# Performance work log

Hardware: AMD Instinct MI355X
Metric: run time of the kernel (lower is better)

The kernel has to match this reference:

```python
import jax, jax.numpy as jnp
import numpy as np

NUM_HEADS = 12

def setup_inputs() -> dict:
    key = jax.random.key(0)
    ks = jax.random.split(key, 4)
    B, N, C = 64, 512, 768
    x = jax.random.normal(ks[0], (B, N, C), dtype=jnp.float32)
    qkv_w = jax.random.normal(ks[1], (3 * C, C), dtype=jnp.float32) * 0.02
    proj_w = jax.random.normal(ks[2], (C, C), dtype=jnp.float32) * 0.02
    proj_b = jnp.zeros((C,), dtype=jnp.float32)
    bias_table = jax.random.normal(ks[3], (2 * N - 1, NUM_HEADS), dtype=jnp.float32) * 0.02
    return {"x": x, "qkv_w": qkv_w, "proj_w": proj_w, "proj_b": proj_b, "bias_table": bias_table}

def reference(x, qkv_w, proj_w, proj_b, bias_table):
    B, N, C = x.shape
    H = NUM_HEADS
    hd = C // H
    scale = hd ** (-0.5)
    # qkv projection (no bias): [B,N,3C] -> [3,B,H,N,hd]
    qkv = (x @ qkv_w.T).reshape(B, N, 3, H, hd)
    qkv = jnp.transpose(qkv, (2, 0, 3, 1, 4))
    q, k, v = qkv[0], qkv[1], qkv[2]
    # relative position bias: rel index in [0, 2N-2]
    coords = jnp.arange(N)
    rel = coords[:, None] - coords[None, :] + (N - 1)  # [N,N]
    bias = jnp.transpose(bias_table[rel], (2, 0, 1))   # [H,N,N]
    attn = jnp.einsum('bhnd,bhmd->bhnm', q, k) * scale + bias[None]
    attn = jax.nn.softmax(attn, axis=-1)
    out = jnp.einsum('bhnm,bhmd->bhnd', attn, v)       # [B,H,N,hd]
    out = jnp.transpose(out, (0, 2, 1, 3)).reshape(B, N, C)
    return out @ proj_w.T + proj_b
```

## Files before the change

kernel.cpp:

```cpp
#include <hip/hip_runtime.h>
#include <hip/hip_bf16.h>

#define DI static __device__ __forceinline__

typedef __attribute__((ext_vector_type(8), may_alias)) short short8;
typedef __attribute__((ext_vector_type(4), may_alias)) short short4a;
typedef __attribute__((ext_vector_type(4), may_alias)) float floatx4a;
typedef __attribute__((ext_vector_type(4))) float floatx4;

constexpr int Bsz = 64, Nseq = 512, Cdim = 768, NH = 12, HD = 64;
constexpr int QS = Bsz * NH * Nseq * HD;
constexpr float QK_PRESCALE = 0.18033688011112042f;
constexpr float LOG2E = 1.4426950408889634f;

DI ushort f2bf(float f) {
  union { float f; unsigned u; } v; v.f = f;
  unsigned r = v.u + 0x7FFF + ((v.u >> 16) & 1);
  return (ushort)(r >> 16);
}
DI float bf2f(ushort u) {
  union { unsigned u; float f; } v; v.u = ((unsigned)u) << 16;
  return v.f;
}

DI void gload_lds16(const ushort* g, ushort* l) {
  __builtin_amdgcn_global_load_lds(
      (const __attribute__((address_space(1))) unsigned int*)g,
      (__attribute__((address_space(3))) unsigned int*)l, 16, 0, 0);
}

__global__ void cvt8(const float* __restrict__ s, ushort* __restrict__ d, int n) {
  int i = (blockIdx.x * 256 + threadIdx.x) * 8;
  if (i >= n) return;
  floatx4a a = *(const floatx4a*)(s + i);
  floatx4a b = *(const floatx4a*)(s + i + 4);
  short8 r;
  r[0] = (short)f2bf(a[0]); r[1] = (short)f2bf(a[1]);
  r[2] = (short)f2bf(a[2]); r[3] = (short)f2bf(a[3]);
  r[4] = (short)f2bf(b[0]); r[5] = (short)f2bf(b[1]);
  r[6] = (short)f2bf(b[2]); r[7] = (short)f2bf(b[3]);
  *(short8*)(d + i) = r;
}
__global__ void cvt1s(const float* __restrict__ s, ushort* __restrict__ d, int n) {
  int i = blockIdx.x * 256 + threadIdx.x;
  if (i < n) d[i] = f2bf(s[i] * LOG2E);
}

__global__ __launch_bounds__(256) void qkv_gemm(
    const ushort* __restrict__ x, const ushort* __restrict__ w,
    ushort* __restrict__ qo, ushort* __restrict__ ko, ushort* __restrict__ vo)
{
  __shared__ __align__(16) ushort As[128 * 64];
  __shared__ __align__(16) ushort Ws[128 * 64];
  const int id = blockIdx.y * 18 + blockIdx.x;
  const int swz = (id & 7) * 576 + (id >> 3);
  const int bm = swz / 18;
  const int bn = swz % 18;
  const int t = threadIdx.x;
  const int wv = t >> 6, ln = t & 63, lq = ln >> 4, lm = ln & 15;
  const int wm = wv >> 1, wn = wv & 1;

  const int srow = wv * 32 + (ln >> 3);
  const int scol = (ln & 7) * 8;

  floatx4 acc[4][4];
  #pragma unroll
  for (int i = 0; i < 4; ++i)
    #pragma unroll
    for (int j = 0; j < 4; ++j) acc[i][j] = (floatx4)0.f;

  for (int kt = 0; kt < Cdim / 64; ++kt) {
    #pragma unroll
    for (int i = 0; i < 4; ++i) {
      gload_lds16(&x[(size_t)(bm * 128 + srow + i * 8) * Cdim + kt * 64 + scol],
                  &As[(wv * 32 + i * 8) * 64]);
      gload_lds16(&w[(size_t)(bn * 128 + srow + i * 8) * Cdim + kt * 64 + scol],
                  &Ws[(wv * 32 + i * 8) * 64]);
    }
    __syncthreads();
    #pragma unroll
    for (int ks = 0; ks < 2; ++ks) {
      short8 af[4], bfr[4];
      #pragma unroll
      for (int i = 0; i < 4; ++i)
        af[i] = *(const short8*)&As[(wm * 64 + i * 16 + lm) * 64 + ks * 32 + lq * 8];
      #pragma unroll
      for (int j = 0; j < 4; ++j)
        bfr[j] = *(const short8*)&Ws[(wn * 64 + j * 16 + lm) * 64 + ks * 32 + lq * 8];
      #pragma unroll
      for (int i = 0; i < 4; ++i)
        #pragma unroll
        for (int j = 0; j < 4; ++j)
          acc[i][j] = __builtin_amdgcn_mfma_f32_16x16x32_bf16(af[i], bfr[j], acc[i][j], 0, 0, 0);
    }
    __syncthreads();
  }

  const int cbase = bn * 128 + wn * 64;
  const int which = cbase / Cdim;
  const int h = (cbase % Cdim) >> 6;
  const float osc = (which == 0) ? QK_PRESCALE : 1.f;
  #pragma unroll
  for (int i = 0; i < 4; ++i) {
    int gm0 = bm * 128 + wm * 64 + i * 16 + lq * 4;
    int b = gm0 >> 9, ns0 = gm0 & 511;
    #pragma unroll
    for (int j = 0; j < 4; ++j) {
      int d = j * 16 + lm;
      if (which == 2) {
        short4a v4;
        #pragma unroll
        for (int r = 0; r < 4; ++r) v4[r] = (short)f2bf(acc[i][j][r]);
        *(short4a*)&vo[(size_t)((b * NH + h) * HD + d) * Nseq + ns0] = v4;
      } else {
        ushort* outp = which == 0 ? qo : ko;
        #pragma unroll
        for (int r = 0; r < 4; ++r)
          outp[(size_t)((b * NH + h) * Nseq + ns0 + r) * HD + d] = f2bf(acc[i][j][r] * osc);
      }
    }
  }
}

__global__ __launch_bounds__(256) void attn_kernel(
    const ushort* __restrict__ q, const ushort* __restrict__ k,
    const ushort* __restrict__ vt, const ushort* __restrict__ bt,
    ushort* __restrict__ ao)
{
  __shared__ __align__(16) ushort Qs[64 * 72];
  __shared__ __align__(16) ushort Ks[64 * 72];
  __shared__ __align__(16) ushort Vs[64 * 72];
  __shared__ __align__(16) ushort Ps[64 * 72];
  __shared__ float biasLds[128];
  const int blk = blockIdx.x;
  const int bh = blk % (Bsz * NH);
  const int qt = blk / (Bsz * NH);
  const int h = bh % NH, b = bh / NH;
  const int t = threadIdx.x;
  const int wv = t >> 6, ln = t & 63, lq = ln >> 4, lm = ln & 15;
  const size_t base = (size_t)bh * (Nseq * HD);

  #pragma unroll
  for (int i = 0; i < 2; ++i) {
    int id = t + 256 * i;
    int r = id >> 3, c = (id & 7) << 3;
    *(short8*)&Qs[r * 72 + c] =
        *(const short8*)&q[base + (size_t)(qt * 64 + r) * HD + c];
  }
  __syncthreads();
  short8 qa[2];
  #pragma unroll
  for (int ks = 0; ks < 2; ++ks)
    qa[ks] = *(const short8*)&Qs[(wv * 16 + lm) * 72 + ks * 32 + lq * 8];

  floatx4 o[4];
  #pragma unroll
  for (int i = 0; i < 4; ++i) o[i] = (floatx4)0.f;
  float lrow[4];
  #pragma unroll
  for (int r = 0; r < 4; ++r) lrow[r] = 0.f;

  for (int kt = 0; kt < Nseq / 64; ++kt) {
    #pragma unroll
    for (int i = 0; i < 2; ++i) {
      int id = t + 256 * i;
      int r = id >> 3, c = (id & 7) << 3;
      *(short8*)&Ks[r * 72 + c] =
          *(const short8*)&k[base + (size_t)(kt * 64 + r) * HD + c];
      *(short8*)&Vs[r * 72 + c] =
          *(const short8*)&vt[base + (size_t)r * Nseq + kt * 64 + c];
    }
    if (t < 127) biasLds[t] = bf2f(bt[(qt * 64 - kt * 64 + 448 + t) * NH + h]);
    __syncthreads();

    floatx4 s[4];
    #pragma unroll
    for (int cb = 0; cb < 4; ++cb) s[cb] = (floatx4)0.f;
    #pragma unroll
    for (int ks = 0; ks < 2; ++ks) {
      #pragma unroll
      for (int cb = 0; cb < 4; ++cb) {
        short8 bfr = *(const short8*)&Ks[(cb * 16 + lm) * 72 + ks * 32 + lq * 8];
        s[cb] = __builtin_amdgcn_mfma_f32_16x16x32_bf16(qa[ks], bfr, s[cb], 0, 0, 0);
      }
    }

    #pragma unroll
    for (int r = 0; r < 4; ++r) {
      int row_in = wv * 16 + lq * 4 + r;
      #pragma unroll
      for (int cb = 0; cb < 4; ++cb) {
        int col_in = cb * 16 + lm;
        float p = __builtin_amdgcn_exp2f(s[cb][r] + biasLds[row_in - col_in + 63]);
        lrow[r] += p;
        Ps[row_in * 72 + col_in] = f2bf(p);
      }
    }
    __syncthreads();

    #pragma unroll
    for (int ks = 0; ks < 2; ++ks) {
      short8 a = *(const short8*)&Ps[(wv * 16 + lm) * 72 + ks * 32 + lq * 8];
      #pragma unroll
      for (int db = 0; db < 4; ++db) {
        short8 bfr = *(const short8*)&Vs[(db * 16 + lm) * 72 + ks * 32 + lq * 8];
        o[db] = __builtin_amdgcn_mfma_f32_16x16x32_bf16(a, bfr, o[db], 0, 0, 0);
      }
    }
    __syncthreads();
  }

  #pragma unroll
  for (int r = 0; r < 4; ++r) {
    #pragma unroll
    for (int off = 8; off; off >>= 1) lrow[r] += __shfl_xor(lrow[r], off);
  }

  #pragma unroll
  for (int r = 0; r < 4; ++r) {
    int qi = qt * 64 + wv * 16 + lq * 4 + r;
    float inv = 1.f / lrow[r];
    #pragma unroll
    for (int db = 0; db < 4; ++db) {
      int d = db * 16 + lm;
      ao[(size_t)(b * Nseq + qi) * Cdim + h * HD + d] = f2bf(o[db][r] * inv);
    }
  }
}

__global__ __launch_bounds__(256) void proj_gemm(
    const ushort* __restrict__ a, const ushort* __restrict__ w,
    const ushort* __restrict__ pb, float* __restrict__ out)
{
  __shared__ __align__(16) ushort As[128 * 64];
  __shared__ __align__(16) ushort Ws[128 * 64];
  const int id = blockIdx.y * 6 + blockIdx.x;
  const int swz = (id & 7) * 192 + (id >> 3);
  const int bm = swz / 6;
  const int bn = swz % 6;
  const int t = threadIdx.x;
  const int wv = t >> 6, ln = t & 63, lq = ln >> 4, lm = ln & 15;
  const int wm = wv >> 1, wn = wv & 1;

  const int srow = wv * 32 + (ln >> 3);
  const int scol = (ln & 7) * 8;

  floatx4 acc[4][4];
  #pragma unroll
  for (int i = 0; i < 4; ++i)
    #pragma unroll
    for (int j = 0; j < 4; ++j) acc[i][j] = (floatx4)0.f;

  for (int kt = 0; kt < Cdim / 64; ++kt) {
    #pragma unroll
    for (int i = 0; i < 4; ++i) {
      gload_lds16(&a[(size_t)(bm * 128 + srow + i * 8) * Cdim + kt * 64 + scol],
                  &As[(wv * 32 + i * 8) * 64]);
      gload_lds16(&w[(size_t)(bn * 128 + srow + i * 8) * Cdim + kt * 64 + scol],
                  &Ws[(wv * 32 + i * 8) * 64]);
    }
    __syncthreads();
    #pragma unroll
    for (int ks = 0; ks < 2; ++ks) {
      short8 af[4], bfr[4];
      #pragma unroll
      for (int i = 0; i < 4; ++i)
        af[i] = *(const short8*)&As[(wm * 64 + i * 16 + lm) * 64 + ks * 32 + lq * 8];
      #pragma unroll
      for (int j = 0; j < 4; ++j)
        bfr[j] = *(const short8*)&Ws[(wn * 64 + j * 16 + lm) * 64 + ks * 32 + lq * 8];
      #pragma unroll
      for (int i = 0; i < 4; ++i)
        #pragma unroll
        for (int j = 0; j < 4; ++j)
          acc[i][j] = __builtin_amdgcn_mfma_f32_16x16x32_bf16(af[i], bfr[j], acc[i][j], 0, 0, 0);
    }
    __syncthreads();
  }

  #pragma unroll
  for (int j = 0; j < 4; ++j) {
    int gn = bn * 128 + wn * 64 + j * 16 + lm;
    float bias = bf2f(pb[gn]);
    #pragma unroll
    for (int i = 0; i < 4; ++i) {
      #pragma unroll
      for (int r = 0; r < 4; ++r) {
        int gm = bm * 128 + wm * 64 + i * 16 + lq * 4 + r;
        out[(size_t)gm * Cdim + gn] = acc[i][j][r] + bias;
      }
    }
  }
}

extern "C" void kernel_launch(void* const* d_in, const int* in_sizes, int n_in,
                              void* d_out, int out_size, void* d_ws, size_t ws_size,
                              hipStream_t stream) {
  const float* x  = (const float*)d_in[0];
  const float* qw = (const float*)d_in[1];
  const float* pw = (const float*)d_in[2];
  const float* pb = (const float*)d_in[3];
  const float* bt = (const float*)d_in[4];
  float* out = (float*)d_out;

  constexpr int NX = Bsz * Nseq * Cdim;
  constexpr int NQW = 3 * Cdim * Cdim;
  constexpr int NPW = Cdim * Cdim;
  constexpr int NBT = (2 * Nseq - 1) * NH;

  ushort* qs  = (ushort*)d_ws;
  ushort* ks  = qs + QS;
  ushort* vts = ks + QS;
  ushort* ao  = vts + QS;
  ushort* xb  = ao;
  ushort* qwb = ao + QS;
  ushort* pwb = qwb + NQW;
  ushort* pbb = pwb + NPW;
  ushort* btb = pbb + Cdim;

  cvt8<<<(NX  + 2047) / 2048, 256, 0, stream>>>(x,  xb,  NX);
  cvt8<<<(NQW + 2047) / 2048, 256, 0, stream>>>(qw, qwb, NQW);
  cvt8<<<(NPW + 2047) / 2048, 256, 0, stream>>>(pw, pwb, NPW);
  cvt8<<<1, 256, 0, stream>>>(pb, pbb, Cdim);
  cvt1s<<<(NBT + 255) / 256, 256, 0, stream>>>(bt, btb, NBT);

  qkv_gemm<<<dim3(18, 256), 256, 0, stream>>>(xb, qwb, qs, ks, vts);
  attn_kernel<<<dim3(Bsz * NH * (Nseq / 64)), 256, 0, stream>>>(qs, ks, vts, btb, ao);
  proj_gemm<<<dim3(6, 256), 256, 0, stream>>>(ao, pwb, pbb, out);
}
```

Baseline: 562.8 us.

## Double-buffer GEMM LDS tiles and enlarge QKV GEMM tiles to 256x256

Both the QKV and projection GEMMs now prefetch the next K-tile into a second LDS buffer while computing on the current one, using explicit vmcnt waits and raw barriers in place of __syncthreads. The QKV GEMM also grows to 256x256 tiles with 512 threads (8 waves, each computing 128x64), so each loaded tile is reused by more MFMA work. This targets global-load latency and lowers load traffic per FLOP. The cost is larger LDS use (128KB for QKV), more accumulator registers, and fewer resident blocks per CU.

Measured after the change: 539.1 us. 4.2% less time.

```diff
diff --git a/kernel.cpp b/kernel.cpp
--- a/kernel.cpp
+++ b/kernel.cpp
@@ -46,63 +46,77 @@
   if (i < n) d[i] = f2bf(s[i] * LOG2E);
 }
 
-__global__ __launch_bounds__(256) void qkv_gemm(
+__global__ __launch_bounds__(512, 2) void qkv_gemm(
     const ushort* __restrict__ x, const ushort* __restrict__ w,
     ushort* __restrict__ qo, ushort* __restrict__ ko, ushort* __restrict__ vo)
 {
-  __shared__ __align__(16) ushort As[128 * 64];
-  __shared__ __align__(16) ushort Ws[128 * 64];
-  const int id = blockIdx.y * 18 + blockIdx.x;
-  const int swz = (id & 7) * 576 + (id >> 3);
-  const int bm = swz / 18;
-  const int bn = swz % 18;
+  __shared__ __align__(16) ushort As[2][256 * 64];
+  __shared__ __align__(16) ushort Ws[2][256 * 64];
+  const int id = blockIdx.y * 9 + blockIdx.x;
+  const int swz = (id & 7) * 144 + (id >> 3);
+  const int bm = swz / 9;
+  const int bn = swz % 9;
   const int t = threadIdx.x;
   const int wv = t >> 6, ln = t & 63, lq = ln >> 4, lm = ln & 15;
-  const int wm = wv >> 1, wn = wv & 1;
-
-  const int srow = wv * 32 + (ln >> 3);
+  const int wm = wv >> 2, wn = wv & 3;
+
+  const int srow = ln >> 3;
   const int scol = (ln & 7) * 8;
 
-  floatx4 acc[4][4];
-  #pragma unroll
-  for (int i = 0; i < 4; ++i)
+  floatx4 acc[8][4];
+  #pragma unroll
+  for (int i = 0; i < 8; ++i)
     #pragma unroll
     for (int j = 0; j < 4; ++j) acc[i][j] = (floatx4)0.f;
 
-  for (int kt = 0; kt < Cdim / 64; ++kt) {
-    #pragma unroll
-    for (int i = 0; i < 4; ++i) {
-      gload_lds16(&x[(size_t)(bm * 128 + srow + i * 8) * Cdim + kt * 64 + scol],
-                  &As[(wv * 32 + i * 8) * 64]);
-      gload_lds16(&w[(size_t)(bn * 128 + srow + i * 8) * Cdim + kt * 64 + scol],
-                  &Ws[(wv * 32 + i * 8) * 64]);
-    }
-    __syncthreads();
+  auto stage = [&](int buf, int kt) {
+    #pragma unroll
+    for (int p = 0; p < 4; ++p) {
+      int c = wv * 4 + p;
+      int row = c * 8 + srow;
+      gload_lds16(&x[(size_t)(bm * 256 + row) * Cdim + kt * 64 + scol],
+                  &As[buf][c * 512]);
+      gload_lds16(&w[(size_t)(bn * 256 + row) * Cdim + kt * 64 + scol],
+                  &Ws[buf][c * 512]);
+    }
+  };
+
+  stage(0, 0);
+  for (int kt = 0; kt < 12; ++kt) {
+    const int cur = kt & 1;
+    if (kt < 11) {
+      stage(cur ^ 1, kt + 1);
+      asm volatile("s_waitcnt vmcnt(8)" ::: "memory");
+    } else {
+      asm volatile("s_waitcnt vmcnt(0)" ::: "memory");
+    }
+    __builtin_amdgcn_s_barrier();
     #pragma unroll
     for (int ks = 0; ks < 2; ++ks) {
-      short8 af[4], bfr[4];
-      #pragma unroll
-      for (int i = 0; i < 4; ++i)
-        af[i] = *(const short8*)&As[(wm * 64 + i * 16 + lm) * 64 + ks * 32 + lq * 8];
+      short8 af[8], bfr[4];
+      #pragma unroll
+      for (int i = 0; i < 8; ++i)
+        af[i] = *(const short8*)&As[cur][(wm * 128 + i * 16 + lm) * 64 + ks * 32 + lq * 8];
       #pragma unroll
       for (int j = 0; j < 4; ++j)
-        bfr[j] = *(const short8*)&Ws[(wn * 64 + j * 16 + lm) * 64 + ks * 32 + lq * 8];
-      #pragma unroll
-      for (int i = 0; i < 4; ++i)
+        bfr[j] = *(const short8*)&Ws[cur][(wn * 64 + j * 16 + lm) * 64 + ks * 32 + lq * 8];
+      #pragma unroll
+      for (int i = 0; i < 8; ++i)
         #pragma unroll
         for (int j = 0; j < 4; ++j)
           acc[i][j] = __builtin_amdgcn_mfma_f32_16x16x32_bf16(af[i], bfr[j], acc[i][j], 0, 0, 0);
     }
-    __syncthreads();
-  }
-
-  const int cbase = bn * 128 + wn * 64;
+    asm volatile("s_waitcnt lgkmcnt(0)" ::: "memory");
+    __builtin_amdgcn_s_barrier();
+  }
+
+  const int cbase = bn * 256 + wn * 64;
   const int which = cbase / Cdim;
   const int h = (cbase % Cdim) >> 6;
   const float osc = (which == 0) ? QK_PRESCALE : 1.f;
   #pragma unroll
-  for (int i = 0; i < 4; ++i) {
-    int gm0 = bm * 128 + wm * 64 + i * 16 + lq * 4;
+  for (int i = 0; i < 8; ++i) {
+    int gm0 = bm * 256 + wm * 128 + i * 16 + lq * 4;
     int b = gm0 >> 9, ns0 = gm0 & 511;
     #pragma unroll
     for (int j = 0; j < 4; ++j) {
@@ -228,12 +242,12 @@
   }
 }
 
-__global__ __launch_bounds__(256) void proj_gemm(
+__global__ __launch_bounds__(256, 2) void proj_gemm(
     const ushort* __restrict__ a, const ushort* __restrict__ w,
     const ushort* __restrict__ pb, float* __restrict__ out)
 {
-  __shared__ __align__(16) ushort As[128 * 64];
-  __shared__ __align__(16) ushort Ws[128 * 64];
+  __shared__ __align__(16) ushort As[2][128 * 64];
+  __shared__ __align__(16) ushort Ws[2][128 * 64];
   const int id = blockIdx.y * 6 + blockIdx.x;
   const int swz = (id & 7) * 192 + (id >> 3);
   const int bm = swz / 6;
@@ -242,7 +256,7 @@
   const int wv = t >> 6, ln = t & 63, lq = ln >> 4, lm = ln & 15;
   const int wm = wv >> 1, wn = wv & 1;
 
-  const int srow = wv * 32 + (ln >> 3);
+  const int srow = ln >> 3;
   const int scol = (ln & 7) * 8;
 
   floatx4 acc[4][4];
@@ -251,31 +265,45 @@
     #pragma unroll
     for (int j = 0; j < 4; ++j) acc[i][j] = (floatx4)0.f;
 
-  for (int kt = 0; kt < Cdim / 64; ++kt) {
-    #pragma unroll
-    for (int i = 0; i < 4; ++i) {
-      gload_lds16(&a[(size_t)(bm * 128 + srow + i * 8) * Cdim + kt * 64 + scol],
-                  &As[(wv * 32 + i * 8) * 64]);
-      gload_lds16(&w[(size_t)(bn * 128 + srow + i * 8) * Cdim + kt * 64 + scol],
-                  &Ws[(wv * 32 + i * 8) * 64]);
-    }
-    __syncthreads();
+  auto stage = [&](int buf, int kt) {
+    #pragma unroll
+    for (int p = 0; p < 4; ++p) {
+      int c = wv * 4 + p;
+      int row = c * 8 + srow;
+      gload_lds16(&a[(size_t)(bm * 128 + row) * Cdim + kt * 64 + scol],
+                  &As[buf][c * 512]);
+      gload_lds16(&w[(size_t)(bn * 128 + row) * Cdim + kt * 64 + scol],
+                  &Ws[buf][c * 512]);
+    }
+  };
+
+  stage(0, 0);
+  for (int kt = 0; kt < 12; ++kt) {
+    const int cur = kt & 1;
+    if (kt < 11) {
+      stage(cur ^ 1, kt + 1);
+      asm volatile("s_waitcnt vmcnt(8)" ::: "memory");
+    } else {
+      asm volatile("s_waitcnt vmcnt(0)" ::: "memory");
+    }
+    __builtin_amdgcn_s_barrier();
     #pragma unroll
     for (int ks = 0; ks < 2; ++ks) {
       short8 af[4], bfr[4];
       #pragma unroll
       for (int i = 0; i < 4; ++i)
-        af[i] = *(const short8*)&As[(wm * 64 + i * 16 + lm) * 64 + ks * 32 + lq * 8];
+        af[i] = *(const short8*)&As[cur][(wm * 64 + i * 16 + lm) * 64 + ks * 32 + lq * 8];
       #pragma unroll
       for (int j = 0; j < 4; ++j)
-        bfr[j] = *(const short8*)&Ws[(wn * 64 + j * 16 + lm) * 64 + ks * 32 + lq * 8];
+        bfr[j] = *(const short8*)&Ws[cur][(wn * 64 + j * 16 + lm) * 64 + ks * 32 + lq * 8];
       #pragma unroll
       for (int i = 0; i < 4; ++i)
         #pragma unroll
         for (int j = 0; j < 4; ++j)
           acc[i][j] = __builtin_amdgcn_mfma_f32_16x16x32_bf16(af[i], bfr[j], acc[i][j], 0, 0, 0);
     }
-    __syncthreads();
+    asm volatile("s_waitcnt lgkmcnt(0)" ::: "memory");
+    __builtin_amdgcn_s_barrier();
   }
 
   #pragma unroll
@@ -324,7 +352,7 @@
   cvt8<<<1, 256, 0, stream>>>(pb, pbb, Cdim);
   cvt1s<<<(NBT + 255) / 256, 256, 0, stream>>>(bt, btb, NBT);
 
-  qkv_gemm<<<dim3(18, 256), 256, 0, stream>>>(xb, qwb, qs, ks, vts);
+  qkv_gemm<<<dim3(9, 128), 512, 0, stream>>>(xb, qwb, qs, ks, vts);
   attn_kernel<<<dim3(Bsz * NH * (Nseq / 64)), 256, 0, stream>>>(qs, ks, vts, btb, ao);
   proj_gemm<<<dim3(6, 256), 256, 0, stream>>>(ao, pwb, pbb, out);
 }
```
